# Performance work log

Hardware: AMD Instinct MI355X
Metric: run time of the kernel (lower is better)

The kernel has to match this reference:

```python
import jax, jax.numpy as jnp
import numpy as np

B, R, N, D_IN, D_OUT = 8, 8, 1024, 256, 256


def setup_inputs() -> dict:
    key = jax.random.key(0)
    k1, k2, k3, k4 = jax.random.split(key, 4)
    x = jax.random.normal(k1, (B, N, D_IN), dtype=jnp.float32)
    adj_stack = jax.random.uniform(k2, (B, R, N, N), dtype=jnp.float32)
    # per-relation Linear params, stacked: W[r] maps D_IN -> D_OUT
    bound = 1.0 / np.sqrt(D_IN)
    W = jax.random.uniform(k3, (R, D_IN, D_OUT), minval=-bound, maxval=bound, dtype=jnp.float32)
    b = jax.random.uniform(k4, (R, D_OUT), minval=-bound, maxval=bound, dtype=jnp.float32)
    return {"x": x, "adj_stack": adj_stack, "W": W, "b": b}


def reference(x, adj_stack, W, b):
    # support[b,r,n,e] = x[b,n,:] @ W[r] + b[r]
    support = jnp.einsum('bnd,rde->brne', x, W) + b[None, :, None, :]
    # out[b,m,e] = sum_r adj[b,r,m,:] @ support[b,r,:,e]
    out = jnp.einsum('brmn,brne->bme', adj_stack, support)
    return jax.nn.relu(out)
```

## Files before the change

kernel.cpp:

```cpp
#include <hip/hip_runtime.h>
#include <hip/hip_bf16.h>


#define Rr 8
#define Nn 1024
#define Dd 256
#define PITCH 40

typedef __attribute__((ext_vector_type(8))) short short8;
typedef __attribute__((ext_vector_type(4))) float f32x4;

__device__ __forceinline__ short f2bf(float f) {
    unsigned u = __builtin_bit_cast(unsigned, f);
    u += 0x7fffu + ((u >> 16) & 1u);
    return (short)(u >> 16);
}

__global__ void prep_w_kernel(const float* __restrict__ W, short* __restrict__ Wt) {
    __shared__ short T[64][72];
    const int tid = threadIdx.x;
    const int et = blockIdx.x, dt = blockIdx.y, r = blockIdx.z;
    const float* Wr = W + ((size_t)r * Dd + dt * 64) * Dd + et * 64;
    #pragma unroll
    for (int i = 0; i < 4; ++i) {
        int idx = tid + i * 256;
        int d_l = idx >> 4;
        int e4  = (idx & 15) * 4;
        f32x4 v = *(const f32x4*)(Wr + d_l * Dd + e4);
        T[e4 + 0][d_l] = f2bf(v[0]);
        T[e4 + 1][d_l] = f2bf(v[1]);
        T[e4 + 2][d_l] = f2bf(v[2]);
        T[e4 + 3][d_l] = f2bf(v[3]);
    }
    __syncthreads();
    short* o = Wt + ((size_t)r * Dd + et * 64) * Dd + dt * 64;
    #pragma unroll
    for (int i = 0; i < 2; ++i) {
        int idx = tid + i * 256;
        *(short8*)(o + (idx >> 3) * Dd + (idx & 7) * 8) = *(const short8*)&T[idx >> 3][(idx & 7) * 8];
    }
}

__global__ __launch_bounds__(256, 3) void support_kernel(
        const float* __restrict__ x, const short* __restrict__ Wt,
        const float* __restrict__ bias, short* __restrict__ sup) {
    __shared__ short As[2][128 * PITCH];
    __shared__ short Bs[2][128 * PITCH];

    const int tid = threadIdx.x;
    const int wave = tid >> 6, lane = tid & 63;
    const int quad = lane >> 4, l16 = lane & 15;
    const int e_t = blockIdx.x, n_t = blockIdx.y, br = blockIdx.z;
    const int b = br >> 3, r = br & 7;
    const int we = wave & 1, wn = wave >> 1;

    const short* wp = Wt + ((size_t)r * Dd + e_t * 128) * Dd;
    const float* xb = x + ((size_t)b * Nn + n_t * 128) * Dd;

    short8 aw[2];
    f32x4 xv[4];
    auto gload = [&](int d0) {
        #pragma unroll
        for (int i = 0; i < 2; ++i) {
            int idx = tid + i * 256;
            aw[i] = *(const short8*)(wp + (idx >> 2) * Dd + d0 + (idx & 3) * 8);
        }
        #pragma unroll
        for (int i = 0; i < 2; ++i) {
            int idx = tid + i * 256;
            const float* p = xb + (idx >> 2) * Dd + d0 + (idx & 3) * 8;
            xv[2 * i]     = *(const f32x4*)p;
            xv[2 * i + 1] = *(const f32x4*)(p + 4);
        }
    };
    auto stage = [&](int buf) {
        #pragma unroll
        for (int i = 0; i < 2; ++i) {
            int idx = tid + i * 256;
            *(short8*)&As[buf][(idx >> 2) * PITCH + (idx & 3) * 8] = aw[i];
        }
        #pragma unroll
        for (int i = 0; i < 2; ++i) {
            int idx = tid + i * 256;
            short8 t;
            t[0] = f2bf(xv[2 * i][0]); t[1] = f2bf(xv[2 * i][1]);
            t[2] = f2bf(xv[2 * i][2]); t[3] = f2bf(xv[2 * i][3]);
            t[4] = f2bf(xv[2 * i + 1][0]); t[5] = f2bf(xv[2 * i + 1][1]);
            t[6] = f2bf(xv[2 * i + 1][2]); t[7] = f2bf(xv[2 * i + 1][3]);
            *(short8*)&Bs[buf][(idx >> 2) * PITCH + (idx & 3) * 8] = t;
        }
    };

    f32x4 acc[4][4] = {};
    gload(0);
    for (int it = 0; it < 8; ++it) {
        const int buf = it & 1;
        stage(buf);
        __syncthreads();
        if (it < 7) gload((it + 1) * 32);
        short8 a[4], bfr[4];
        #pragma unroll
        for (int i = 0; i < 4; ++i)
            a[i] = *(const short8*)&As[buf][(we * 64 + i * 16 + l16) * PITCH + quad * 8];
        #pragma unroll
        for (int j = 0; j < 4; ++j)
            bfr[j] = *(const short8*)&Bs[buf][(wn * 64 + j * 16 + l16) * PITCH + quad * 8];
        #pragma unroll
        for (int i = 0; i < 4; ++i)
            #pragma unroll
            for (int j = 0; j < 4; ++j)
                acc[i][j] = __builtin_amdgcn_mfma_f32_16x16x32_bf16(a[i], bfr[j], acc[i][j], 0, 0, 0);
    }

    #pragma unroll
    for (int i = 0; i < 4; ++i)
        #pragma unroll
        for (int reg = 0; reg < 4; ++reg) {
            int e = e_t * 128 + we * 64 + i * 16 + quad * 4 + reg;
            float bv = bias[r * Dd + e];
            #pragma unroll
            for (int j = 0; j < 4; ++j) {
                int n = n_t * 128 + wn * 64 + j * 16 + l16;
                sup[(((b * Rr + r) * Dd + e) << 10) + n] = f2bf(acc[i][j][reg] + bv);
            }
        }
}

__global__ __launch_bounds__(256, 3) void gcn_gemm_kernel(
        const float* __restrict__ adj, const short* __restrict__ sup,
        float* __restrict__ out) {
    __shared__ short Aa[2][128 * PITCH];
    __shared__ short Bs[2][128 * PITCH];

    const int tid = threadIdx.x;
    const int wave = tid >> 6, lane = tid & 63;
    const int quad = lane >> 4, l16 = lane & 15;
    const int r = blockIdx.x & 7, e2 = blockIdx.x >> 3;
    const int m_t = blockIdx.y, b = blockIdx.z;
    const int wm = wave >> 1, we = wave & 1;

    const float* ap = adj + ((size_t)((b * Rr + r) * Nn + m_t * 128)) * Nn;
    const short* bp = sup + (((size_t)((b * Rr + r) * Dd + e2 * 128)) << 10);

    f32x4 av[4];
    short8 bv[2];
    auto gload = [&](int kk) {
        #pragma unroll
        for (int i = 0; i < 2; ++i) {
            int idx = tid + i * 256;
            const float* p = ap + (size_t)(idx >> 2) * Nn + kk + (idx & 3) * 8;
            av[2 * i]     = *(const f32x4*)p;
            av[2 * i + 1] = *(const f32x4*)(p + 4);
        }
        #pragma unroll
        for (int i = 0; i < 2; ++i) {
            int idx = tid + i * 256;
            bv[i] = *(const short8*)(bp + ((size_t)(idx >> 2) << 10) + kk + (idx & 3) * 8);
        }
    };
    auto stage = [&](int buf) {
        #pragma unroll
        for (int i = 0; i < 2; ++i) {
            int idx = tid + i * 256;
            short8 t;
            t[0] = f2bf(av[2 * i][0]); t[1] = f2bf(av[2 * i][1]);
            t[2] = f2bf(av[2 * i][2]); t[3] = f2bf(av[2 * i][3]);
            t[4] = f2bf(av[2 * i + 1][0]); t[5] = f2bf(av[2 * i + 1][1]);
            t[6] = f2bf(av[2 * i + 1][2]); t[7] = f2bf(av[2 * i + 1][3]);
            *(short8*)&Aa[buf][(idx >> 2) * PITCH + (idx & 3) * 8] = t;
        }
        #pragma unroll
        for (int i = 0; i < 2; ++i) {
            int idx = tid + i * 256;
            *(short8*)&Bs[buf][(idx >> 2) * PITCH + (idx & 3) * 8] = bv[i];
        }
    };

    f32x4 acc[4][4] = {};
    gload(0);
    for (int it = 0; it < 32; ++it) {
        const int buf = it & 1;
        stage(buf);
        __syncthreads();
        if (it < 31) gload((it + 1) * 32);
        short8 a[4], bfr[4];
        #pragma unroll
        for (int i = 0; i < 4; ++i)
            a[i] = *(const short8*)&Aa[buf][(wm * 64 + i * 16 + l16) * PITCH + quad * 8];
        #pragma unroll
        for (int j = 0; j < 4; ++j)
            bfr[j] = *(const short8*)&Bs[buf][(we * 64 + j * 16 + l16) * PITCH + quad * 8];
        #pragma unroll
        for (int i = 0; i < 4; ++i)
            #pragma unroll
            for (int j = 0; j < 4; ++j)
                acc[i][j] = __builtin_amdgcn_mfma_f32_16x16x32_bf16(a[i], bfr[j], acc[i][j], 0, 0, 0);
    }

    float* ob = out + ((size_t)b * Nn + m_t * 128) * Dd + e2 * 128;
    #pragma unroll
    for (int i = 0; i < 4; ++i)
        #pragma unroll
        for (int reg = 0; reg < 4; ++reg) {
            int m_l = wm * 64 + i * 16 + quad * 4 + reg;
            #pragma unroll
            for (int j = 0; j < 4; ++j)
                atomicAdd(ob + (size_t)m_l * Dd + we * 64 + j * 16 + l16, acc[i][j][reg]);
        }
}

__global__ void relu_kernel(float* __restrict__ out, int n4) {
    int i = blockIdx.x * blockDim.x + threadIdx.x;
    if (i < n4) {
        f32x4* p = (f32x4*)out;
        f32x4 v = p[i];
        v[0] = fmaxf(v[0], 0.f); v[1] = fmaxf(v[1], 0.f);
        v[2] = fmaxf(v[2], 0.f); v[3] = fmaxf(v[3], 0.f);
        p[i] = v;
    }
}

extern "C" void kernel_launch(void* const* d_in, const int* in_sizes, int n_in,
                              void* d_out, int out_size, void* d_ws, size_t ws_size,
                              hipStream_t stream) {
    const float* x    = (const float*)d_in[0];
    const float* adj  = (const float*)d_in[1];
    const float* W    = (const float*)d_in[2];
    const float* bias = (const float*)d_in[3];
    float* out = (float*)d_out;
    short* sup = (short*)d_ws;
    short* Wt  = (short*)d_out;

    prep_w_kernel<<<dim3(4, 4, 8), 256, 0, stream>>>(W, Wt);
    support_kernel<<<dim3(2, 8, 64), 256, 0, stream>>>(x, Wt, bias, sup);
    hipMemsetAsync(d_out, 0, (size_t)out_size * sizeof(float), stream);
    gcn_gemm_kernel<<<dim3(16, 8, 8), 256, 0, stream>>>(adj, sup, out);
    relu_kernel<<<(out_size / 4 + 255) / 256, 256, 0, stream>>>(out, out_size / 4);
}
```

Baseline: 461.3 us.

## Drop LDS staging for single-wave direct-load GEMMs and replace atomics with partial-sum reduction

```diff
diff --git a/kernel.cpp b/kernel.cpp
--- a/kernel.cpp
+++ b/kernel.cpp
@@ -5,7 +5,6 @@
 #define Rr 8
 #define Nn 1024
 #define Dd 256
-#define PITCH 40
 
 typedef __attribute__((ext_vector_type(8))) short short8;
 typedef __attribute__((ext_vector_type(4))) float f32x4;
@@ -14,6 +13,13 @@
     unsigned u = __builtin_bit_cast(unsigned, f);
     u += 0x7fffu + ((u >> 16) & 1u);
     return (short)(u >> 16);
+}
+
+__device__ __forceinline__ short8 cvt8(f32x4 lo, f32x4 hi) {
+    short8 t;
+    t[0] = f2bf(lo[0]); t[1] = f2bf(lo[1]); t[2] = f2bf(lo[2]); t[3] = f2bf(lo[3]);
+    t[4] = f2bf(hi[0]); t[5] = f2bf(hi[1]); t[6] = f2bf(hi[2]); t[7] = f2bf(hi[3]);
+    return t;
 }
 
 __global__ void prep_w_kernel(const float* __restrict__ W, short* __restrict__ Wt) {
@@ -41,70 +47,33 @@
     }
 }
 
-__global__ __launch_bounds__(256, 3) void support_kernel(
+__global__ __launch_bounds__(64, 3) void support_kernel(
         const float* __restrict__ x, const short* __restrict__ Wt,
         const float* __restrict__ bias, short* __restrict__ sup) {
-    __shared__ short As[2][128 * PITCH];
-    __shared__ short Bs[2][128 * PITCH];
+    const int lane = threadIdx.x;
+    const int quad = lane >> 4, l16 = lane & 15;
+    const int bid = blockIdx.x;
+    const int b   = bid & 7;
+    const int e_t = (bid >> 3) & 3;
+    const int n_t = (bid >> 5) & 15;
+    const int r   = bid >> 9;
 
-    const int tid = threadIdx.x;
-    const int wave = tid >> 6, lane = tid & 63;
-    const int quad = lane >> 4, l16 = lane & 15;
-    const int e_t = blockIdx.x, n_t = blockIdx.y, br = blockIdx.z;
-    const int b = br >> 3, r = br & 7;
-    const int we = wave & 1, wn = wave >> 1;
-
-    const short* wp = Wt + ((size_t)r * Dd + e_t * 128) * Dd;
-    const float* xb = x + ((size_t)b * Nn + n_t * 128) * Dd;
-
-    short8 aw[2];
-    f32x4 xv[4];
-    auto gload = [&](int d0) {
-        #pragma unroll
-        for (int i = 0; i < 2; ++i) {
-            int idx = tid + i * 256;
-            aw[i] = *(const short8*)(wp + (idx >> 2) * Dd + d0 + (idx & 3) * 8);
-        }
-        #pragma unroll
-        for (int i = 0; i < 2; ++i) {
-            int idx = tid + i * 256;
-            const float* p = xb + (idx >> 2) * Dd + d0 + (idx & 3) * 8;
-            xv[2 * i]     = *(const f32x4*)p;
-            xv[2 * i + 1] = *(const f32x4*)(p + 4);
-        }
-    };
-    auto stage = [&](int buf) {
-        #pragma unroll
-        for (int i = 0; i < 2; ++i) {
-            int idx = tid + i * 256;
-            *(short8*)&As[buf][(idx >> 2) * PITCH + (idx & 3) * 8] = aw[i];
-        }
-        #pragma unroll
-        for (int i = 0; i < 2; ++i) {
-            int idx = tid + i * 256;
-            short8 t;
-            t[0] = f2bf(xv[2 * i][0]); t[1] = f2bf(xv[2 * i][1]);
-            t[2] = f2bf(xv[2 * i][2]); t[3] = f2bf(xv[2 * i][3]);
-            t[4] = f2bf(xv[2 * i + 1][0]); t[5] = f2bf(xv[2 * i + 1][1]);
-            t[6] = f2bf(xv[2 * i + 1][2]); t[7] = f2bf(xv[2 * i + 1][3]);
-            *(short8*)&Bs[buf][(idx >> 2) * PITCH + (idx & 3) * 8] = t;
-        }
-    };
+    const short* wp = Wt + ((size_t)r * Dd + e_t * 64) * Dd;
+    const float* xb = x + ((size_t)b * Nn + n_t * 64) * Dd;
 
     f32x4 acc[4][4] = {};
-    gload(0);
-    for (int it = 0; it < 8; ++it) {
-        const int buf = it & 1;
-        stage(buf);
-        __syncthreads();
-        if (it < 7) gload((it + 1) * 32);
+    #pragma unroll 2
+    for (int kt = 0; kt < 8; ++kt) {
+        const int d0 = kt * 32;
         short8 a[4], bfr[4];
         #pragma unroll
         for (int i = 0; i < 4; ++i)
-            a[i] = *(const short8*)&As[buf][(we * 64 + i * 16 + l16) * PITCH + quad * 8];
+            a[i] = *(const short8*)(wp + (i * 16 + l16) * Dd + d0 + quad * 8);
         #pragma unroll
-        for (int j = 0; j < 4; ++j)
-            bfr[j] = *(const short8*)&Bs[buf][(wn * 64 + j * 16 + l16) * PITCH + quad * 8];
+        for (int j = 0; j < 4; ++j) {
+            const float* p = xb + (j * 16 + l16) * Dd + d0 + quad * 8;
+            bfr[j] = cvt8(*(const f32x4*)p, *(const f32x4*)(p + 4));
+        }
         #pragma unroll
         for (int i = 0; i < 4; ++i)
             #pragma unroll
@@ -116,108 +85,76 @@
     for (int i = 0; i < 4; ++i)
         #pragma unroll
         for (int reg = 0; reg < 4; ++reg) {
-            int e = e_t * 128 + we * 64 + i * 16 + quad * 4 + reg;
+            int e = e_t * 64 + i * 16 + quad * 4 + reg;
             float bv = bias[r * Dd + e];
             #pragma unroll
             for (int j = 0; j < 4; ++j) {
-                int n = n_t * 128 + wn * 64 + j * 16 + l16;
+                int n = n_t * 64 + j * 16 + l16;
                 sup[(((b * Rr + r) * Dd + e) << 10) + n] = f2bf(acc[i][j][reg] + bv);
             }
         }
 }
 
-__global__ __launch_bounds__(256, 3) void gcn_gemm_kernel(
+__global__ __launch_bounds__(64, 4) void gcn_gemm_kernel(
         const float* __restrict__ adj, const short* __restrict__ sup,
-        float* __restrict__ out) {
-    __shared__ short Aa[2][128 * PITCH];
-    __shared__ short Bs[2][128 * PITCH];
+        float* __restrict__ part) {
+    const int lane = threadIdx.x;
+    const int quad = lane >> 4, l16 = lane & 15;
+    const int bid = blockIdx.x;
+    const int r   = bid & 7;
+    const int e_t = (bid >> 3) & 3;
+    const int m_t = (bid >> 5) & 31;
+    const int b   = bid >> 10;
 
-    const int tid = threadIdx.x;
-    const int wave = tid >> 6, lane = tid & 63;
-    const int quad = lane >> 4, l16 = lane & 15;
-    const int r = blockIdx.x & 7, e2 = blockIdx.x >> 3;
-    const int m_t = blockIdx.y, b = blockIdx.z;
-    const int wm = wave >> 1, we = wave & 1;
+    const float* ap = adj + ((size_t)((b * Rr + r) * Nn + m_t * 32)) * Nn;
+    const short* bp = sup + (((size_t)((b * Rr + r) * Dd + e_t * 64)) << 10);
 
-    const float* ap = adj + ((size_t)((b * Rr + r) * Nn + m_t * 128)) * Nn;
-    const short* bp = sup + (((size_t)((b * Rr + r) * Dd + e2 * 128)) << 10);
-
-    f32x4 av[4];
-    short8 bv[2];
-    auto gload = [&](int kk) {
+    f32x4 acc[2][4] = {};
+    #pragma unroll 2
+    for (int kt = 0; kt < 32; ++kt) {
+        const int k0 = kt * 32;
+        short8 a[2], bfr[4];
         #pragma unroll
         for (int i = 0; i < 2; ++i) {
-            int idx = tid + i * 256;
-            const float* p = ap + (size_t)(idx >> 2) * Nn + kk + (idx & 3) * 8;
-            av[2 * i]     = *(const f32x4*)p;
-            av[2 * i + 1] = *(const f32x4*)(p + 4);
+            const float* p = ap + (size_t)(i * 16 + l16) * Nn + k0 + quad * 8;
+            a[i] = cvt8(*(const f32x4*)p, *(const f32x4*)(p + 4));
         }
         #pragma unroll
-        for (int i = 0; i < 2; ++i) {
-            int idx = tid + i * 256;
-            bv[i] = *(const short8*)(bp + ((size_t)(idx >> 2) << 10) + kk + (idx & 3) * 8);
-        }
-    };
-    auto stage = [&](int buf) {
+        for (int j = 0; j < 4; ++j)
+            bfr[j] = *(const short8*)(bp + ((size_t)(j * 16 + l16) << 10) + k0 + quad * 8);
         #pragma unroll
-        for (int i = 0; i < 2; ++i) {
-            int idx = tid + i * 256;
-            short8 t;
-            t[0] = f2bf(av[2 * i][0]); t[1] = f2bf(av[2 * i][1]);
-            t[2] = f2bf(av[2 * i][2]); t[3] = f2bf(av[2 * i][3]);
-            t[4] = f2bf(av[2 * i + 1][0]); t[5] = f2bf(av[2 * i + 1][1]);
-            t[6] = f2bf(av[2 * i + 1][2]); t[7] = f2bf(av[2 * i + 1][3]);
-            *(short8*)&Aa[buf][(idx >> 2) * PITCH + (idx & 3) * 8] = t;
-        }
-        #pragma unroll
-        for (int i = 0; i < 2; ++i) {
-            int idx = tid + i * 256;
-            *(short8*)&Bs[buf][(idx >> 2) * PITCH + (idx & 3) * 8] = bv[i];
-        }
-    };
-
-    f32x4 acc[4][4] = {};
-    gload(0);
-    for (int it = 0; it < 32; ++it) {
-        const int buf = it & 1;
-        stage(buf);
-        __syncthreads();
-        if (it < 31) gload((it + 1) * 32);
-        short8 a[4], bfr[4];
-        #pragma unroll
-        for (int i = 0; i < 4; ++i)
-            a[i] = *(const short8*)&Aa[buf][(wm * 64 + i * 16 + l16) * PITCH + quad * 8];
-        #pragma unroll
-        for (int j = 0; j < 4; ++j)
-            bfr[j] = *(const short8*)&Bs[buf][(we * 64 + j * 16 + l16) * PITCH + quad * 8];
-        #pragma unroll
-        for (int i = 0; i < 4; ++i)
+        for (int i = 0; i < 2; ++i)
             #pragma unroll
             for (int j = 0; j < 4; ++j)
                 acc[i][j] = __builtin_amdgcn_mfma_f32_16x16x32_bf16(a[i], bfr[j], acc[i][j], 0, 0, 0);
     }
 
-    float* ob = out + ((size_t)b * Nn + m_t * 128) * Dd + e2 * 128;
+    float* pr = part + ((size_t)r << 21) + ((size_t)b * Nn + m_t * 32) * Dd + e_t * 64;
     #pragma unroll
-    for (int i = 0; i < 4; ++i)
+    for (int i = 0; i < 2; ++i)
         #pragma unroll
         for (int reg = 0; reg < 4; ++reg) {
-            int m_l = wm * 64 + i * 16 + quad * 4 + reg;
+            int m_l = i * 16 + quad * 4 + reg;
             #pragma unroll
             for (int j = 0; j < 4; ++j)
-                atomicAdd(ob + (size_t)m_l * Dd + we * 64 + j * 16 + l16, acc[i][j][reg]);
+                pr[(size_t)m_l * Dd + j * 16 + l16] = acc[i][j][reg];
         }
 }
 
-__global__ void relu_kernel(float* __restrict__ out, int n4) {
+__global__ __launch_bounds__(256) void reduce_relu_kernel(
+        const float* __restrict__ part, float* __restrict__ out, int n4) {
     int i = blockIdx.x * blockDim.x + threadIdx.x;
-    if (i < n4) {
-        f32x4* p = (f32x4*)out;
-        f32x4 v = p[i];
-        v[0] = fmaxf(v[0], 0.f); v[1] = fmaxf(v[1], 0.f);
-        v[2] = fmaxf(v[2], 0.f); v[3] = fmaxf(v[3], 0.f);
-        p[i] = v;
+    if (i >= n4) return;
+    const f32x4* p = (const f32x4*)part;
+    f32x4 v = p[i];
+    #pragma unroll
+    for (int k = 1; k < 8; ++k) {
+        f32x4 t = p[i + ((size_t)k << 19)];
+        v[0] += t[0]; v[1] += t[1]; v[2] += t[2]; v[3] += t[3];
     }
+    v[0] = fmaxf(v[0], 0.f); v[1] = fmaxf(v[1], 0.f);
+    v[2] = fmaxf(v[2], 0.f); v[3] = fmaxf(v[3], 0.f);
+    ((f32x4*)out)[i] = v;
 }
 
 extern "C" void kernel_launch(void* const* d_in, const int* in_sizes, int n_in,
@@ -228,12 +165,12 @@
     const float* W    = (const float*)d_in[2];
     const float* bias = (const float*)d_in[3];
     float* out = (float*)d_out;
-    short* sup = (short*)d_ws;
-    short* Wt  = (short*)d_out;
+    short* sup  = (short*)d_ws;
+    float* part = (float*)((char*)d_ws + (32u << 20));
+    short* Wt   = (short*)d_out;
 
     prep_w_kernel<<<dim3(4, 4, 8), 256, 0, stream>>>(W, Wt);
-    support_kernel<<<dim3(2, 8, 64), 256, 0, stream>>>(x, Wt, bias, sup);
-    hipMemsetAsync(d_out, 0, (size_t)out_size * sizeof(float), stream);
-    gcn_gemm_kernel<<<dim3(16, 8, 8), 256, 0, stream>>>(adj, sup, out);
-    relu_kernel<<<(out_size / 4 + 255) / 256, 256, 0, stream>>>(out, out_size / 4);
+    support_kernel<<<4096, 64, 0, stream>>>(x, Wt, bias, sup);
+    gcn_gemm_kernel<<<8192, 64, 0, stream>>>(adj, sup, part);
+    reduce_relu_kernel<<<(out_size / 4 + 255) / 256, 256, 0, stream>>>(part, out, out_size / 4);
 }
```

After: 592.2 us. 28.4% more time.
